# Optimization experiments

Hardware: AMD Instinct MI355X
Metric: run time of the kernel (lower is better)

## Reference

```python
import jax, jax.numpy as jnp
import numpy as np

WINDOW = (8, 8)
NUM_HEADS = 6
PAD_H, PAD_W = WINDOW[0] // 2, WINDOW[1] // 2


def window_partition(x, wh, ww):
    # x: (B, C, H, W) -> (B*nh*nw, wh*ww, C)
    B, C, H, W = x.shape
    nh, nw = H // wh, W // ww
    x = x.reshape(B, C, nh, wh, nw, ww)
    x = x.transpose(0, 2, 4, 3, 5, 1)  # B, nh, nw, wh, ww, C
    return x.reshape(B * nh * nw, wh * ww, C)


def window_merge(x, B, C, H, W, wh, ww):
    # x: (B*nh*nw, wh*ww, C) -> (B, C, H, W)
    nh, nw = H // wh, W // ww
    x = x.reshape(B, nh, nw, wh, ww, C)
    x = x.transpose(0, 5, 1, 3, 2, 4)  # B, C, nh, wh, nw, ww
    return x.reshape(B, C, H, W)


def window_mha(t, num_heads):
    # t: (Bn, N, 3*C) packed qkv -> (Bn, N, C)
    Bn, N, C3 = t.shape
    C = C3 // 3
    d = C // num_heads
    q, k, v = jnp.split(t, 3, axis=-1)
    to_heads = lambda u: u.reshape(Bn, N, num_heads, d).transpose(0, 2, 1, 3)
    q, k, v = to_heads(q), to_heads(k), to_heads(v)
    scale = 1.0 / np.sqrt(d)
    attn = jax.nn.softmax(jnp.einsum('bhnd,bhmd->bhnm', q, k) * scale, axis=-1)
    o = jnp.einsum('bhnm,bhmd->bhnd', attn, v)
    return o.transpose(0, 2, 1, 3).reshape(Bn, N, C)


def setup_inputs() -> dict:
    key = jax.random.key(0)
    ks = jax.random.split(key, 5)
    B, C, H, W = 4, 384, 128, 128
    Cq = 64 * NUM_HEADS  # qkv_dim * num_heads = 384
    return {
        'x': jax.random.normal(ks[0], (B, C, H, W), dtype=jnp.float32),
        'w_qkv': jax.random.normal(ks[1], (3 * Cq, C), dtype=jnp.float32) * 0.02,
        'b_qkv': jax.random.normal(ks[2], (3 * Cq,), dtype=jnp.float32) * 0.02,
        'w_head': jax.random.normal(ks[3], (C, Cq), dtype=jnp.float32) * 0.02,
        'b_head': jax.random.normal(ks[4], (C,), dtype=jnp.float32) * 0.02,
    }


def reference(x, w_qkv, b_qkv, w_head, b_head):
    B, C, H, W = x.shape
    wh, ww = WINDOW
    # 1x1 conv qkv projection
    qkv = jnp.einsum('bchw,oc->bohw', x, w_qkv) + b_qkv[None, :, None, None]
    Cq = qkv.shape[1] // 3
    # branch 1: unpadded windows
    x1 = window_partition(qkv, wh, ww)
    x1 = window_mha(x1, NUM_HEADS)
    x1 = window_merge(x1, B, Cq, H, W, wh, ww)
    # branch 2: pad by half window, windows, then crop back
    qkv_p = jnp.pad(qkv, ((0, 0), (0, 0), (PAD_H, PAD_H), (PAD_W, PAD_W)))
    Hp, Wp = H + 2 * PAD_H, W + 2 * PAD_W
    x2 = window_partition(qkv_p, wh, ww)
    x2 = window_mha(x2, NUM_HEADS)
    x2 = window_merge(x2, B, Cq, Hp, Wp, wh, ww)
    x2 = x2[:, :, PAD_H:Hp - PAD_H, PAD_W:Wp - PAD_W]
    # merge + 1x1 conv head projection
    out = jnp.einsum('bchw,oc->bohw', x1 + x2, w_head) + b_head[None, :, None, None]
    return out
```

## Files before the change

kernel.cpp:

```cpp
#include <hip/hip_runtime.h>

typedef __bf16 bf16x8 __attribute__((ext_vector_type(8)));
typedef float f32x4 __attribute__((ext_vector_type(4)));

#define HW 16384
#define SP 66

union U4B8 { uint4 u; bf16x8 v; __bf16 h[8]; };
union U2B4 { uint2 u; __bf16 h[4]; };

__device__ __forceinline__ void gload_lds16(const __bf16* g, __bf16* l) {
    __builtin_amdgcn_global_load_lds(
        (const __attribute__((address_space(1))) unsigned int*)g,
        (__attribute__((address_space(3))) unsigned int*)l, 16, 0, 0);
}

__global__ __launch_bounds__(256) void k_xt(const float* __restrict__ x,
    __bf16* __restrict__ xT)
{
    __shared__ __bf16 T[64 * 68];
    const int tid = threadIdx.x;
    const int hw0 = blockIdx.x * 64;
    const int c0  = blockIdx.y * 64;
    const int b   = blockIdx.z;
    const float* xb = x + (size_t)b * 384 * HW;
#pragma unroll
    for (int it = 0; it < 4; ++it) {
        int unit = it * 256 + tid;
        int c = unit >> 4, q = unit & 15;
        float4 f = *(const float4*)(xb + (size_t)(c0 + c) * HW + hw0 + q * 4);
        U2B4 t;
        t.h[0] = (__bf16)f.x; t.h[1] = (__bf16)f.y;
        t.h[2] = (__bf16)f.z; t.h[3] = (__bf16)f.w;
        *(uint2*)(T + c * 68 + q * 4) = t.u;
    }
    __syncthreads();
    __bf16* xtb = xT + (size_t)b * HW * 384;
#pragma unroll
    for (int it = 0; it < 2; ++it) {
        int unit = it * 256 + tid;
        int hw = unit >> 3, c8 = unit & 7;
        U4B8 t;
#pragma unroll
        for (int j = 0; j < 8; ++j) t.h[j] = T[(c8 * 8 + j) * 68 + hw];
        *(uint4*)(xtb + (size_t)(hw0 + hw) * 384 + c0 + c8 * 8) = t.u;
    }
}

__global__ __launch_bounds__(256) void k_cvt(const float* __restrict__ src,
    __bf16* __restrict__ dst)
{
    int idx = (blockIdx.x * 256 + threadIdx.x) * 8;
    float4 f0 = *(const float4*)(src + idx);
    float4 f1 = *(const float4*)(src + idx + 4);
    U4B8 t;
    t.h[0] = (__bf16)f0.x; t.h[1] = (__bf16)f0.y;
    t.h[2] = (__bf16)f0.z; t.h[3] = (__bf16)f0.w;
    t.h[4] = (__bf16)f1.x; t.h[5] = (__bf16)f1.y;
    t.h[6] = (__bf16)f1.z; t.h[7] = (__bf16)f1.w;
    *(uint4*)(dst + idx) = t.u;
}

__global__ __launch_bounds__(256) void k_qkv(const __bf16* __restrict__ xT,
    const __bf16* __restrict__ wqb, const float* __restrict__ bq,
    __bf16* __restrict__ qk, __bf16* __restrict__ vT)
{
    __shared__ __bf16 As[2][128 * 64];
    __shared__ __bf16 Bs[2][128 * 64];
    const int tid = threadIdx.x;
    const int hw0 = blockIdx.x * 128;
    const int o0  = blockIdx.y * 128;
    const int b   = blockIdx.z;

    f32x4 acc[4][4];
#pragma unroll
    for (int i = 0; i < 4; ++i)
#pragma unroll
        for (int j = 0; j < 4; ++j)
#pragma unroll
            for (int e = 0; e < 4; ++e) acc[i][j][e] = 0.0f;

    const int l = tid & 63;
    const int wv = tid >> 6;
    const int wm = wv & 1;
    const int wn = wv >> 1;
    const int l16 = l & 15, quad = l >> 4;

    const __bf16* wrow = wqb + (size_t)o0 * 384;
    const __bf16* xrow = xT + (size_t)b * HW * 384 + (size_t)hw0 * 384;
    const int r = tid >> 3, c8 = (tid & 7) * 8;

    auto STAGE = [&](int buf, int kt) {
        const int c0 = kt * 64;
#pragma unroll
        for (int it = 0; it < 4; ++it) {
            int unit = it * 256 + tid;
            int rr = r + it * 32;
            gload_lds16(wrow + (size_t)rr * 384 + c0 + c8, &As[buf][unit * 8]);
            gload_lds16(xrow + (size_t)rr * 384 + c0 + c8, &Bs[buf][unit * 8]);
        }
    };

    STAGE(0, 0);
    __syncthreads();
    int cur = 0;
    for (int kt = 0; kt < 6; ++kt) {
        if (kt < 5) STAGE(cur ^ 1, kt + 1);
#pragma unroll
        for (int ks = 0; ks < 2; ++ks) {
            bf16x8 a[4], bb[4];
#pragma unroll
            for (int t = 0; t < 4; ++t)
                a[t] = *(const bf16x8*)(&As[cur][(wm * 64 + t * 16 + l16) * 64 + ks * 32 + quad * 8]);
#pragma unroll
            for (int t = 0; t < 4; ++t)
                bb[t] = *(const bf16x8*)(&Bs[cur][(wn * 64 + t * 16 + l16) * 64 + ks * 32 + quad * 8]);
#pragma unroll
            for (int mt = 0; mt < 4; ++mt)
#pragma unroll
                for (int nt = 0; nt < 4; ++nt)
                    acc[mt][nt] = __builtin_amdgcn_mfma_f32_16x16x32_bf16(
                        a[mt], bb[nt], acc[mt][nt], 0, 0, 0);
        }
        if (kt < 5) __syncthreads();
        cur ^= 1;
    }

    if (o0 < 768) {
        __bf16* qb = qk + (size_t)b * HW * 768;
#pragma unroll
        for (int mt = 0; mt < 4; ++mt) {
            int oo = o0 + wm * 64 + mt * 16 + quad * 4;
            float4 bias = *(const float4*)(bq + oo);
#pragma unroll
            for (int nt = 0; nt < 4; ++nt) {
                int hw = hw0 + wn * 64 + nt * 16 + l16;
                U2B4 t;
                t.h[0] = (__bf16)(acc[mt][nt][0] + bias.x);
                t.h[1] = (__bf16)(acc[mt][nt][1] + bias.y);
                t.h[2] = (__bf16)(acc[mt][nt][2] + bias.z);
                t.h[3] = (__bf16)(acc[mt][nt][3] + bias.w);
                *(uint2*)(qb + (size_t)hw * 768 + oo) = t.u;
            }
        }
    } else {
        __bf16* vb = vT + (size_t)b * 384 * HW;
#pragma unroll
        for (int mt = 0; mt < 4; ++mt) {
            int oo = o0 + wm * 64 + mt * 16 + quad * 4;
            float4 bias = *(const float4*)(bq + oo);
            int vo = oo - 768;
#pragma unroll
            for (int nt = 0; nt < 4; ++nt) {
                int hw = hw0 + wn * 64 + nt * 16 + l16;
                vb[(size_t)(vo + 0) * HW + hw] = (__bf16)(acc[mt][nt][0] + bias.x);
                vb[(size_t)(vo + 1) * HW + hw] = (__bf16)(acc[mt][nt][1] + bias.y);
                vb[(size_t)(vo + 2) * HW + hw] = (__bf16)(acc[mt][nt][2] + bias.z);
                vb[(size_t)(vo + 3) * HW + hw] = (__bf16)(acc[mt][nt][3] + bias.w);
            }
        }
    }
}

__global__ __launch_bounds__(192) void k_attn1(const __bf16* __restrict__ qk,
    const __bf16* __restrict__ vT, __bf16* __restrict__ y1)
{
    __shared__ __bf16 sm[3][64 * SP];
    const int tid = threadIdx.x;
    const int l = tid & 63, wv = tid >> 6;
    const int wid = blockIdx.x * 3 + wv;
    const int head = wid % 6;
    const int win = wid / 6;
    const int wx = win & 15;
    const int wy = (win >> 4) & 15;
    const int b  = win >> 8;
    const int h0 = wy * 8, w0 = wx * 8;
    const __bf16* qb = qk + (size_t)b * HW * 768;
    const __bf16* vb = vT + (size_t)b * 384 * HW;
    __bf16* P = &sm[wv][0];
    const int l16 = l & 15, quad = l >> 4;
    const int cbase = head * 64;

    size_t toff[4];
#pragma unroll
    for (int t = 0; t < 4; ++t) {
        int tok = t * 16 + l16;
        toff[t] = (size_t)((h0 + (tok >> 3)) * 128 + w0 + (tok & 7)) * 768;
    }

    f32x4 s[4][4];
#pragma unroll
    for (int i = 0; i < 4; ++i)
#pragma unroll
        for (int j = 0; j < 4; ++j)
#pragma unroll
            for (int e = 0; e < 4; ++e) s[i][j][e] = 0.0f;

#pragma unroll
    for (int ks = 0; ks < 2; ++ks) {
        bf16x8 aq[4], bk[4];
#pragma unroll
        for (int t = 0; t < 4; ++t) {
            U4B8 uq, uk;
            uq.u = *(const uint4*)(qb + toff[t] + cbase + ks * 32 + quad * 8);
            uk.u = *(const uint4*)(qb + toff[t] + 384 + cbase + ks * 32 + quad * 8);
            aq[t] = uq.v;
            bk[t] = uk.v;
        }
        __builtin_amdgcn_s_setprio(1);
#pragma unroll
        for (int mt = 0; mt < 4; ++mt)
#pragma unroll
            for (int nt = 0; nt < 4; ++nt)
                s[mt][nt] = __builtin_amdgcn_mfma_f32_16x16x32_bf16(
                    aq[mt], bk[nt], s[mt][nt], 0, 0, 0);
        __builtin_amdgcn_s_setprio(0);
    }

    U4B8 vreg[2][4];
#pragma unroll
    for (int ks = 0; ks < 2; ++ks) {
        const int hh2 = h0 + ks * 4 + quad;
#pragma unroll
        for (int t = 0; t < 4; ++t)
            vreg[ks][t].u = *(const uint4*)(vb +
                (size_t)(cbase + t * 16 + l16) * HW + (hh2 * 128 + w0));
    }

#pragma unroll
    for (int mt = 0; mt < 4; ++mt) {
#pragma unroll
        for (int e = 0; e < 4; ++e) {
            float p[4];
#pragma unroll
            for (int nt = 0; nt < 4; ++nt) p[nt] = __expf(s[mt][nt][e] * 0.125f);
            float sum = (p[0] + p[1]) + (p[2] + p[3]);
#pragma unroll
            for (int st = 1; st < 16; st <<= 1) sum += __shfl_xor(sum, st, 64);
            float r = __fdividef(1.0f, sum);
            int row = mt * 16 + quad * 4 + e;
#pragma unroll
            for (int nt = 0; nt < 4; ++nt)
                P[row * SP + nt * 16 + l16] = (__bf16)(p[nt] * r);
        }
    }

    f32x4 o[4][4];
#pragma unroll
    for (int i = 0; i < 4; ++i)
#pragma unroll
        for (int j = 0; j < 4; ++j)
#pragma unroll
            for (int e = 0; e < 4; ++e) o[i][j][e] = 0.0f;

#pragma unroll
    for (int ks = 0; ks < 2; ++ks) {
        bf16x8 ap[4];
#pragma unroll
        for (int t = 0; t < 4; ++t)
            ap[t] = *(const bf16x8*)(P + (t * 16 + l16) * SP + ks * 32 + quad * 8);
        __builtin_amdgcn_s_setprio(1);
#pragma unroll
        for (int mt = 0; mt < 4; ++mt)
#pragma unroll
            for (int nt = 0; nt < 4; ++nt)
                o[mt][nt] = __builtin_amdgcn_mfma_f32_16x16x32_bf16(
                    ap[mt], vreg[ks][nt].v, o[mt][nt], 0, 0, 0);
        __builtin_amdgcn_s_setprio(0);
    }

#pragma unroll
    for (int mt = 0; mt < 4; ++mt)
#pragma unroll
        for (int e = 0; e < 4; ++e) {
            int row = mt * 16 + quad * 4 + e;
#pragma unroll
            for (int nt = 0; nt < 4; ++nt)
                P[row * SP + nt * 16 + l16] = (__bf16)o[mt][nt][e];
        }

    __bf16* yb = y1 + (size_t)b * HW * 384;
#pragma unroll
    for (int it = 0; it < 8; ++it) {
        int unit = it * 64 + l;
        int tok = unit >> 3, c8 = unit & 7;
        int hh = h0 + (tok >> 3), ww = w0 + (tok & 7);
        *(uint4*)(yb + (size_t)(hh * 128 + ww) * 384 + cbase + c8 * 8) =
            *(const uint4*)(P + tok * SP + c8 * 8);
    }
}

__global__ __launch_bounds__(192) void k_attn2(const __bf16* __restrict__ qk,
    const __bf16* __restrict__ vT, const __bf16* __restrict__ y1,
    __bf16* __restrict__ ysum)
{
    __shared__ __bf16 sm[3][64 * SP];
    const int tid = threadIdx.x;
    const int l = tid & 63, wv = tid >> 6;
    const int wid = blockIdx.x * 3 + wv;
    const int head = wid % 6;
    const int win = wid / 6;
    const int wx = win % 17;
    const int t2 = win / 17;
    const int wy = t2 % 17;
    const int b  = t2 / 17;
    const int h0 = wy * 8 - 4;
    const int w0 = wx * 8 - 4;
    const __bf16* qb = qk + (size_t)b * HW * 768;
    const __bf16* vb = vT + (size_t)b * 384 * HW;
    __bf16* P = &sm[wv][0];
    const int l16 = l & 15, quad = l >> 4;
    const int cbase = head * 64;

    size_t toff[4]; bool tval[4];
#pragma unroll
    for (int t = 0; t < 4; ++t) {
        int tok = t * 16 + l16;
        int hh = h0 + (tok >> 3), ww = w0 + (tok & 7);
        tval[t] = ((unsigned)hh < 128u && (unsigned)ww < 128u);
        toff[t] = tval[t] ? (size_t)(hh * 128 + ww) * 768 : 0;
    }

    f32x4 s[4][4];
#pragma unroll
    for (int i = 0; i < 4; ++i)
#pragma unroll
        for (int j = 0; j < 4; ++j)
#pragma unroll
            for (int e = 0; e < 4; ++e) s[i][j][e] = 0.0f;

#pragma unroll
    for (int ks = 0; ks < 2; ++ks) {
        bf16x8 aq[4], bk[4];
#pragma unroll
        for (int t = 0; t < 4; ++t) {
            U4B8 uq, uk;
            if (tval[t]) {
                uq.u = *(const uint4*)(qb + toff[t] + cbase + ks * 32 + quad * 8);
                uk.u = *(const uint4*)(qb + toff[t] + 384 + cbase + ks * 32 + quad * 8);
            } else {
                uq.u = make_uint4(0, 0, 0, 0);
                uk.u = make_uint4(0, 0, 0, 0);
            }
            aq[t] = uq.v;
            bk[t] = uk.v;
        }
        __builtin_amdgcn_s_setprio(1);
#pragma unroll
        for (int mt = 0; mt < 4; ++mt)
#pragma unroll
            for (int nt = 0; nt < 4; ++nt)
                s[mt][nt] = __builtin_amdgcn_mfma_f32_16x16x32_bf16(
                    aq[mt], bk[nt], s[mt][nt], 0, 0, 0);
        __builtin_amdgcn_s_setprio(0);
    }

    U4B8 vreg[2][4];
#pragma unroll
    for (int ks = 0; ks < 2; ++ks) {
        const int hh2 = h0 + ks * 4 + quad;
        const bool rowok = ((unsigned)hh2 < 128u);
#pragma unroll
        for (int t = 0; t < 4; ++t) {
            U4B8 u;
            u.u = make_uint4(0, 0, 0, 0);
            if (rowok) {
                const __bf16* vp = vb + (size_t)(cbase + t * 16 + l16) * HW
                                   + (hh2 * 128 + w0);
                if (w0 >= 0)   *(uint2*)&u.h[0] = *(const uint2*)vp;
                if (w0 <= 120) *(uint2*)&u.h[4] = *(const uint2*)(vp + 4);
            }
            vreg[ks][t] = u;
        }
    }

#pragma unroll
    for (int mt = 0; mt < 4; ++mt) {
#pragma unroll
        for (int e = 0; e < 4; ++e) {
            float p[4];
#pragma unroll
            for (int nt = 0; nt < 4; ++nt) p[nt] = __expf(s[mt][nt][e] * 0.125f);
            float sum = (p[0] + p[1]) + (p[2] + p[3]);
#pragma unroll
            for (int st = 1; st < 16; st <<= 1) sum += __shfl_xor(sum, st, 64);
            float r = __fdividef(1.0f, sum);
            int row = mt * 16 + quad * 4 + e;
#pragma unroll
            for (int nt = 0; nt < 4; ++nt)
                P[row * SP + nt * 16 + l16] = (__bf16)(p[nt] * r);
        }
    }

    f32x4 o[4][4];
#pragma unroll
    for (int i = 0; i < 4; ++i)
#pragma unroll
        for (int j = 0; j < 4; ++j)
#pragma unroll
            for (int e = 0; e < 4; ++e) o[i][j][e] = 0.0f;

#pragma unroll
    for (int ks = 0; ks < 2; ++ks) {
        bf16x8 ap[4];
#pragma unroll
        for (int t = 0; t < 4; ++t)
            ap[t] = *(const bf16x8*)(P + (t * 16 + l16) * SP + ks * 32 + quad * 8);
        __builtin_amdgcn_s_setprio(1);
#pragma unroll
        for (int mt = 0; mt < 4; ++mt)
#pragma unroll
            for (int nt = 0; nt < 4; ++nt)
                o[mt][nt] = __builtin_amdgcn_mfma_f32_16x16x32_bf16(
                    ap[mt], vreg[ks][nt].v, o[mt][nt], 0, 0, 0);
        __builtin_amdgcn_s_setprio(0);
    }

#pragma unroll
    for (int mt = 0; mt < 4; ++mt)
#pragma unroll
        for (int e = 0; e < 4; ++e) {
            int row = mt * 16 + quad * 4 + e;
#pragma unroll
            for (int nt = 0; nt < 4; ++nt)
                P[row * SP + nt * 16 + l16] = (__bf16)o[mt][nt][e];
        }

    const __bf16* y1b = y1 + (size_t)b * HW * 384;
    __bf16* yb = ysum + (size_t)b * HW * 384;
#pragma unroll
    for (int it = 0; it < 8; ++it) {
        int unit = it * 64 + l;
        int tok = unit >> 3, c8 = unit & 7;
        int hh = h0 + (tok >> 3), ww = w0 + (tok & 7);
        if ((unsigned)hh < 128u && (unsigned)ww < 128u) {
            size_t off = (size_t)(hh * 128 + ww) * 384 + cbase + c8 * 8;
            U4B8 t1, t2, r;
            t1.u = *(const uint4*)(y1b + off);
            t2.u = *(const uint4*)(P + tok * SP + c8 * 8);
#pragma unroll
            for (int e = 0; e < 8; ++e)
                r.h[e] = (__bf16)((float)t1.h[e] + (float)t2.h[e]);
            *(uint4*)(yb + off) = r.u;
        }
    }
}

__global__ __launch_bounds__(256) void k_head(const __bf16* __restrict__ ysum,
    const __bf16* __restrict__ whb, const float* __restrict__ bh,
    float* __restrict__ out)
{
    __shared__ __bf16 As[2][128 * 64];
    __shared__ __bf16 Bs[2][128 * 64];
    const int tid = threadIdx.x;
    const int hw0 = blockIdx.x * 128;
    const int o0  = blockIdx.y * 128;
    const int b   = blockIdx.z;

    f32x4 acc[4][4];
#pragma unroll
    for (int i = 0; i < 4; ++i)
#pragma unroll
        for (int j = 0; j < 4; ++j)
#pragma unroll
            for (int e = 0; e < 4; ++e) acc[i][j][e] = 0.0f;

    const int l = tid & 63, wv = tid >> 6;
    const int wm = wv & 1;
    const int wn = wv >> 1;
    const int l16 = l & 15, quad = l >> 4;

    const __bf16* yrow = ysum + (size_t)b * HW * 384 + (size_t)hw0 * 384;
    const __bf16* wrow = whb + (size_t)o0 * 384;
    const int r = tid >> 3, c8 = (tid & 7) * 8;

    auto STAGE = [&](int buf, int kt) {
        const int c0 = kt * 64;
#pragma unroll
        for (int it = 0; it < 4; ++it) {
            int unit = it * 256 + tid;
            int rr = r + it * 32;
            gload_lds16(yrow + (size_t)rr * 384 + c0 + c8, &As[buf][unit * 8]);
            gload_lds16(wrow + (size_t)rr * 384 + c0 + c8, &Bs[buf][unit * 8]);
        }
    };

    STAGE(0, 0);
    __syncthreads();
    int cur = 0;
    for (int kt = 0; kt < 6; ++kt) {
        if (kt < 5) STAGE(cur ^ 1, kt + 1);
#pragma unroll
        for (int ks = 0; ks < 2; ++ks) {
            bf16x8 a[4], bb[4];
#pragma unroll
            for (int t = 0; t < 4; ++t)
                a[t] = *(const bf16x8*)(&As[cur][(wm * 64 + t * 16 + l16) * 64 + ks * 32 + quad * 8]);
#pragma unroll
            for (int t = 0; t < 4; ++t)
                bb[t] = *(const bf16x8*)(&Bs[cur][(wn * 64 + t * 16 + l16) * 64 + ks * 32 + quad * 8]);
#pragma unroll
            for (int mt = 0; mt < 4; ++mt)
#pragma unroll
                for (int nt = 0; nt < 4; ++nt)
                    acc[mt][nt] = __builtin_amdgcn_mfma_f32_16x16x32_bf16(
                        a[mt], bb[nt], acc[mt][nt], 0, 0, 0);
        }
        if (kt < 5) __syncthreads();
        cur ^= 1;
    }

#pragma unroll
    for (int nt = 0; nt < 4; ++nt) {
        int oo = o0 + wn * 64 + nt * 16 + l16;
        float bb_ = bh[oo];
        float* ob = out + ((size_t)b * 384 + oo) * HW + hw0 + wm * 64;
#pragma unroll
        for (int mt = 0; mt < 4; ++mt) {
            float4 f;
            f.x = acc[mt][nt][0] + bb_;
            f.y = acc[mt][nt][1] + bb_;
            f.z = acc[mt][nt][2] + bb_;
            f.w = acc[mt][nt][3] + bb_;
            *(float4*)(ob + mt * 16 + quad * 4) = f;
        }
    }
}

extern "C" void kernel_launch(void* const* d_in, const int* in_sizes, int n_in,
                              void* d_out, int out_size, void* d_ws, size_t ws_size,
                              hipStream_t stream) {
    const float* x  = (const float*)d_in[0];
    const float* wq = (const float*)d_in[1];
    const float* bq = (const float*)d_in[2];
    const float* wh = (const float*)d_in[3];
    const float* bh = (const float*)d_in[4];
    float* out = (float*)d_out;

    __bf16* qk = (__bf16*)d_ws;
    __bf16* vT = qk + (size_t)4 * HW * 768;
    __bf16* y1 = vT + (size_t)4 * 384 * HW;
    __bf16* ys = y1 + (size_t)4 * HW * 384;
    __bf16* xT   = y1;
    __bf16* wqb  = ys;
    __bf16* whb  = vT;

    k_xt   <<<dim3(256, 6, 4), 256, 0, stream>>>(x, xT);
    k_cvt  <<<dim3(216),       256, 0, stream>>>(wq, wqb);
    k_qkv  <<<dim3(128, 9, 4), 256, 0, stream>>>(xT, wqb, bq, qk, vT);
    k_attn1<<<dim3(2048),      192, 0, stream>>>(qk, vT, y1);
    k_attn2<<<dim3(2312),      192, 0, stream>>>(qk, vT, y1, ys);
    k_cvt  <<<dim3(72),        256, 0, stream>>>(wh, whb);
    k_head <<<dim3(128, 3, 4), 256, 0, stream>>>(ys, whb, bh, out);
}
```

Before: 463.2 us.

## Fuse prep kernels, shrink GEMM K-tile, remap blocks for XCDs, hoist V loads

Merges the x-transpose and w_qkv conversion into one k_prep launch. The QKV and head GEMMs now use 32-wide K tiles with 12 stages, which halves LDS use and may raise occupancy. They also raise MFMA priority with s_setprio and remap block IDs so each group of 8 consecutive physical blocks (likely one per XCD) takes a contiguous slice of the logical work. Both attention kernels issue their V loads before the QK^T MFMAs to hide latency. The risks are more barriers per GEMM and different L2 locality.

Result: no change. 458.8 us (-1.0%).

```diff
diff --git a/kernel.cpp b/kernel.cpp
--- a/kernel.cpp
+++ b/kernel.cpp
@@ -15,35 +15,49 @@
         (__attribute__((address_space(3))) unsigned int*)l, 16, 0, 0);
 }
 
-__global__ __launch_bounds__(256) void k_xt(const float* __restrict__ x,
-    __bf16* __restrict__ xT)
+__global__ __launch_bounds__(256) void k_prep(const float* __restrict__ x,
+    __bf16* __restrict__ xT, const float* __restrict__ wq,
+    __bf16* __restrict__ wqb)
 {
     __shared__ __bf16 T[64 * 68];
     const int tid = threadIdx.x;
-    const int hw0 = blockIdx.x * 64;
-    const int c0  = blockIdx.y * 64;
-    const int b   = blockIdx.z;
-    const float* xb = x + (size_t)b * 384 * HW;
-#pragma unroll
-    for (int it = 0; it < 4; ++it) {
-        int unit = it * 256 + tid;
-        int c = unit >> 4, q = unit & 15;
-        float4 f = *(const float4*)(xb + (size_t)(c0 + c) * HW + hw0 + q * 4);
-        U2B4 t;
-        t.h[0] = (__bf16)f.x; t.h[1] = (__bf16)f.y;
-        t.h[2] = (__bf16)f.z; t.h[3] = (__bf16)f.w;
-        *(uint2*)(T + c * 68 + q * 4) = t.u;
-    }
-    __syncthreads();
-    __bf16* xtb = xT + (size_t)b * HW * 384;
-#pragma unroll
-    for (int it = 0; it < 2; ++it) {
-        int unit = it * 256 + tid;
-        int hw = unit >> 3, c8 = unit & 7;
+    const int bid = blockIdx.x;
+    if (bid < 6144) {
+        const int hw0 = (bid & 255) * 64;
+        const int c0  = ((bid >> 8) % 6) * 64;
+        const int b   = bid / 1536;
+        const float* xb = x + (size_t)b * 384 * HW;
+#pragma unroll
+        for (int it = 0; it < 4; ++it) {
+            int unit = it * 256 + tid;
+            int c = unit >> 4, q = unit & 15;
+            float4 f = *(const float4*)(xb + (size_t)(c0 + c) * HW + hw0 + q * 4);
+            U2B4 t;
+            t.h[0] = (__bf16)f.x; t.h[1] = (__bf16)f.y;
+            t.h[2] = (__bf16)f.z; t.h[3] = (__bf16)f.w;
+            *(uint2*)(T + c * 68 + q * 4) = t.u;
+        }
+        __syncthreads();
+        __bf16* xtb = xT + (size_t)b * HW * 384;
+#pragma unroll
+        for (int it = 0; it < 2; ++it) {
+            int unit = it * 256 + tid;
+            int hw = unit >> 3, c8 = unit & 7;
+            U4B8 t;
+#pragma unroll
+            for (int j = 0; j < 8; ++j) t.h[j] = T[(c8 * 8 + j) * 68 + hw];
+            *(uint4*)(xtb + (size_t)(hw0 + hw) * 384 + c0 + c8 * 8) = t.u;
+        }
+    } else {
+        int idx = ((bid - 6144) * 256 + tid) * 8;
+        float4 f0 = *(const float4*)(wq + idx);
+        float4 f1 = *(const float4*)(wq + idx + 4);
         U4B8 t;
-#pragma unroll
-        for (int j = 0; j < 8; ++j) t.h[j] = T[(c8 * 8 + j) * 68 + hw];
-        *(uint4*)(xtb + (size_t)(hw0 + hw) * 384 + c0 + c8 * 8) = t.u;
+        t.h[0] = (__bf16)f0.x; t.h[1] = (__bf16)f0.y;
+        t.h[2] = (__bf16)f0.z; t.h[3] = (__bf16)f0.w;
+        t.h[4] = (__bf16)f1.x; t.h[5] = (__bf16)f1.y;
+        t.h[6] = (__bf16)f1.z; t.h[7] = (__bf16)f1.w;
+        *(uint4*)(wqb + idx) = t.u;
     }
 }
 
@@ -65,12 +79,15 @@
     const __bf16* __restrict__ wqb, const float* __restrict__ bq,
     __bf16* __restrict__ qk, __bf16* __restrict__ vT)
 {
-    __shared__ __bf16 As[2][128 * 64];
-    __shared__ __bf16 Bs[2][128 * 64];
+    __shared__ __bf16 As[2][128 * 32];
+    __shared__ __bf16 Bs[2][128 * 32];
     const int tid = threadIdx.x;
-    const int hw0 = blockIdx.x * 128;
-    const int o0  = blockIdx.y * 128;
-    const int b   = blockIdx.z;
+    const int phys = blockIdx.x;
+    const int logical = (phys & 7) * 576 + (phys >> 3);
+    const int o0  = (logical % 9) * 128;
+    const int rest = logical / 9;
+    const int hw0 = (rest & 127) * 128;
+    const int b   = rest >> 7;
 
     f32x4 acc[4][4];
 #pragma unroll
@@ -88,14 +105,14 @@
 
     const __bf16* wrow = wqb + (size_t)o0 * 384;
     const __bf16* xrow = xT + (size_t)b * HW * 384 + (size_t)hw0 * 384;
-    const int r = tid >> 3, c8 = (tid & 7) * 8;
+    const int r = tid >> 2, c8 = (tid & 3) * 8;
 
     auto STAGE = [&](int buf, int kt) {
-        const int c0 = kt * 64;
-#pragma unroll
-        for (int it = 0; it < 4; ++it) {
+        const int c0 = kt * 32;
+#pragma unroll
+        for (int it = 0; it < 2; ++it) {
             int unit = it * 256 + tid;
-            int rr = r + it * 32;
+            int rr = r + it * 64;
             gload_lds16(wrow + (size_t)rr * 384 + c0 + c8, &As[buf][unit * 8]);
             gload_lds16(xrow + (size_t)rr * 384 + c0 + c8, &Bs[buf][unit * 8]);
         }
@@ -104,25 +121,24 @@
     STAGE(0, 0);
     __syncthreads();
     int cur = 0;
-    for (int kt = 0; kt < 6; ++kt) {
-        if (kt < 5) STAGE(cur ^ 1, kt + 1);
-#pragma unroll
-        for (int ks = 0; ks < 2; ++ks) {
-            bf16x8 a[4], bb[4];
-#pragma unroll
-            for (int t = 0; t < 4; ++t)
-                a[t] = *(const bf16x8*)(&As[cur][(wm * 64 + t * 16 + l16) * 64 + ks * 32 + quad * 8]);
-#pragma unroll
-            for (int t = 0; t < 4; ++t)
-                bb[t] = *(const bf16x8*)(&Bs[cur][(wn * 64 + t * 16 + l16) * 64 + ks * 32 + quad * 8]);
-#pragma unroll
-            for (int mt = 0; mt < 4; ++mt)
-#pragma unroll
-                for (int nt = 0; nt < 4; ++nt)
-                    acc[mt][nt] = __builtin_amdgcn_mfma_f32_16x16x32_bf16(
-                        a[mt], bb[nt], acc[mt][nt], 0, 0, 0);
-        }
-        if (kt < 5) __syncthreads();
+    for (int kt = 0; kt < 12; ++kt) {
+        if (kt < 11) STAGE(cur ^ 1, kt + 1);
+        bf16x8 a[4], bb[4];
+#pragma unroll
+        for (int t = 0; t < 4; ++t)
+            a[t] = *(const bf16x8*)(&As[cur][(wm * 64 + t * 16 + l16) * 32 + quad * 8]);
+#pragma unroll
+        for (int t = 0; t < 4; ++t)
+            bb[t] = *(const bf16x8*)(&Bs[cur][(wn * 64 + t * 16 + l16) * 32 + quad * 8]);
+        __builtin_amdgcn_s_setprio(1);
+#pragma unroll
+        for (int mt = 0; mt < 4; ++mt)
+#pragma unroll
+            for (int nt = 0; nt < 4; ++nt)
+                acc[mt][nt] = __builtin_amdgcn_mfma_f32_16x16x32_bf16(
+                    a[mt], bb[nt], acc[mt][nt], 0, 0, 0);
+        __builtin_amdgcn_s_setprio(0);
+        if (kt < 11) __syncthreads();
         cur ^= 1;
     }
 
@@ -181,6 +197,16 @@
     const int l16 = l & 15, quad = l >> 4;
     const int cbase = head * 64;
 
+    U4B8 vreg[2][4];
+#pragma unroll
+    for (int ks = 0; ks < 2; ++ks) {
+        const int hh2 = h0 + ks * 4 + quad;
+#pragma unroll
+        for (int t = 0; t < 4; ++t)
+            vreg[ks][t].u = *(const uint4*)(vb +
+                (size_t)(cbase + t * 16 + l16) * HW + (hh2 * 128 + w0));
+    }
+
     size_t toff[4];
 #pragma unroll
     for (int t = 0; t < 4; ++t) {
@@ -215,16 +241,6 @@
                 s[mt][nt] = __builtin_amdgcn_mfma_f32_16x16x32_bf16(
                     aq[mt], bk[nt], s[mt][nt], 0, 0, 0);
         __builtin_amdgcn_s_setprio(0);
-    }
-
-    U4B8 vreg[2][4];
-#pragma unroll
-    for (int ks = 0; ks < 2; ++ks) {
-        const int hh2 = h0 + ks * 4 + quad;
-#pragma unroll
-        for (int t = 0; t < 4; ++t)
-            vreg[ks][t].u = *(const uint4*)(vb +
-                (size_t)(cbase + t * 16 + l16) * HW + (hh2 * 128 + w0));
     }
 
 #pragma unroll
@@ -312,6 +328,25 @@
     const int l16 = l & 15, quad = l >> 4;
     const int cbase = head * 64;
 
+    U4B8 vreg[2][4];
+#pragma unroll
+    for (int ks = 0; ks < 2; ++ks) {
+        const int hh2 = h0 + ks * 4 + quad;
+        const bool rowok = ((unsigned)hh2 < 128u);
+#pragma unroll
+        for (int t = 0; t < 4; ++t) {
+            U4B8 u;
+            u.u = make_uint4(0, 0, 0, 0);
+            if (rowok) {
+                const __bf16* vp = vb + (size_t)(cbase + t * 16 + l16) * HW
+                                   + (hh2 * 128 + w0);
+                if (w0 >= 0)   *(uint2*)&u.h[0] = *(const uint2*)vp;
+                if (w0 <= 120) *(uint2*)&u.h[4] = *(const uint2*)(vp + 4);
+            }
+            vreg[ks][t] = u;
+        }
+    }
+
     size_t toff[4]; bool tval[4];
 #pragma unroll
     for (int t = 0; t < 4; ++t) {
@@ -355,25 +390,6 @@
         __builtin_amdgcn_s_setprio(0);
     }
 
-    U4B8 vreg[2][4];
-#pragma unroll
-    for (int ks = 0; ks < 2; ++ks) {
-        const int hh2 = h0 + ks * 4 + quad;
-        const bool rowok = ((unsigned)hh2 < 128u);
-#pragma unroll
-        for (int t = 0; t < 4; ++t) {
-            U4B8 u;
-            u.u = make_uint4(0, 0, 0, 0);
-            if (rowok) {
-                const __bf16* vp = vb + (size_t)(cbase + t * 16 + l16) * HW
-                                   + (hh2 * 128 + w0);
-                if (w0 >= 0)   *(uint2*)&u.h[0] = *(const uint2*)vp;
-                if (w0 <= 120) *(uint2*)&u.h[4] = *(const uint2*)(vp + 4);
-            }
-            vreg[ks][t] = u;
-        }
-    }
-
 #pragma unroll
     for (int mt = 0; mt < 4; ++mt) {
 #pragma unroll
@@ -450,12 +466,15 @@
     const __bf16* __restrict__ whb, const float* __restrict__ bh,
     float* __restrict__ out)
 {
-    __shared__ __bf16 As[2][128 * 64];
-    __shared__ __bf16 Bs[2][128 * 64];
+    __shared__ __bf16 As[2][128 * 32];
+    __shared__ __bf16 Bs[2][128 * 32];
     const int tid = threadIdx.x;
-    const int hw0 = blockIdx.x * 128;
-    const int o0  = blockIdx.y * 128;
-    const int b   = blockIdx.z;
+    const int phys = blockIdx.x;
+    const int logical = (phys & 7) * 192 + (phys >> 3);
+    const int o0  = (logical % 3) * 128;
+    const int rest = logical / 3;
+    const int hw0 = (rest & 127) * 128;
+    const int b   = rest >> 7;
 
     f32x4 acc[4][4];
 #pragma unroll
@@ -472,14 +491,14 @@
 
     const __bf16* yrow = ysum + (size_t)b * HW * 384 + (size_t)hw0 * 384;
     const __bf16* wrow = whb + (size_t)o0 * 384;
-    const int r = tid >> 3, c8 = (tid & 7) * 8;
+    const int r = tid >> 2, c8 = (tid & 3) * 8;
 
     auto STAGE = [&](int buf, int kt) {
-        const int c0 = kt * 64;
-#pragma unroll
-        for (int it = 0; it < 4; ++it) {
+        const int c0 = kt * 32;
+#pragma unroll
+        for (int it = 0; it < 2; ++it) {
             int unit = it * 256 + tid;
-            int rr = r + it * 32;
+            int rr = r + it * 64;
             gload_lds16(yrow + (size_t)rr * 384 + c0 + c8, &As[buf][unit * 8]);
             gload_lds16(wrow + (size_t)rr * 384 + c0 + c8, &Bs[buf][unit * 8]);
         }
@@ -488,25 +507,24 @@
     STAGE(0, 0);
     __syncthreads();
     int cur = 0;
-    for (int kt = 0; kt < 6; ++kt) {
-        if (kt < 5) STAGE(cur ^ 1, kt + 1);
-#pragma unroll
-        for (int ks = 0; ks < 2; ++ks) {
-            bf16x8 a[4], bb[4];
-#pragma unroll
-            for (int t = 0; t < 4; ++t)
-                a[t] = *(const bf16x8*)(&As[cur][(wm * 64 + t * 16 + l16) * 64 + ks * 32 + quad * 8]);
-#pragma unroll
-            for (int t = 0; t < 4; ++t)
-                bb[t] = *(const bf16x8*)(&Bs[cur][(wn * 64 + t * 16 + l16) * 64 + ks * 32 + quad * 8]);
-#pragma unroll
-            for (int mt = 0; mt < 4; ++mt)
-#pragma unroll
-                for (int nt = 0; nt < 4; ++nt)
-                    acc[mt][nt] = __builtin_amdgcn_mfma_f32_16x16x32_bf16(
-                        a[mt], bb[nt], acc[mt][nt], 0, 0, 0);
-        }
-        if (kt < 5) __syncthreads();
+    for (int kt = 0; kt < 12; ++kt) {
+        if (kt < 11) STAGE(cur ^ 1, kt + 1);
+        bf16x8 a[4], bb[4];
+#pragma unroll
+        for (int t = 0; t < 4; ++t)
+            a[t] = *(const bf16x8*)(&As[cur][(wm * 64 + t * 16 + l16) * 32 + quad * 8]);
+#pragma unroll
+        for (int t = 0; t < 4; ++t)
+            bb[t] = *(const bf16x8*)(&Bs[cur][(wn * 64 + t * 16 + l16) * 32 + quad * 8]);
+        __builtin_amdgcn_s_setprio(1);
+#pragma unroll
+        for (int mt = 0; mt < 4; ++mt)
+#pragma unroll
+            for (int nt = 0; nt < 4; ++nt)
+                acc[mt][nt] = __builtin_amdgcn_mfma_f32_16x16x32_bf16(
+                    a[mt], bb[nt], acc[mt][nt], 0, 0, 0);
+        __builtin_amdgcn_s_setprio(0);
+        if (kt < 11) __syncthreads();
         cur ^= 1;
     }
 
@@ -545,11 +563,10 @@
     __bf16* wqb  = ys;
     __bf16* whb  = vT;
 
-    k_xt   <<<dim3(256, 6, 4), 256, 0, stream>>>(x, xT);
-    k_cvt  <<<dim3(216),       256, 0, stream>>>(wq, wqb);
-    k_qkv  <<<dim3(128, 9, 4), 256, 0, stream>>>(xT, wqb, bq, qk, vT);
-    k_attn1<<<dim3(2048),      192, 0, stream>>>(qk, vT, y1);
-    k_attn2<<<dim3(2312),      192, 0, stream>>>(qk, vT, y1, ys);
-    k_cvt  <<<dim3(72),        256, 0, stream>>>(wh, whb);
-    k_head <<<dim3(128, 3, 4), 256, 0, stream>>>(ys, whb, bh, out);
-}
+    k_prep <<<dim3(6360), 256, 0, stream>>>(x, xT, wq, wqb);
+    k_qkv  <<<dim3(4608), 256, 0, stream>>>(xT, wqb, bq, qk, vT);
+    k_attn1<<<dim3(2048), 192, 0, stream>>>(qk, vT, y1);
+    k_attn2<<<dim3(2312), 192, 0, stream>>>(qk, vT, y1, ys);
+    k_cvt  <<<dim3(72),   256, 0, stream>>>(wh, whb);
+    k_head <<<dim3(1536), 256, 0, stream>>>(ys, whb, bh, out);
+}
```
